# Optimization experiments

Hardware: AMD Instinct MI355X
Metric: run time of the kernel (lower is better)

## Reference

```python
import jax, jax.numpy as jnp
import numpy as np

GATE_DECAY = 3.0

def setup_inputs() -> dict:
    key = jax.random.key(0)
    ks = jax.random.split(key, 4)
    B, S, D, I = 8, 2048, 512, 2048
    x = jax.random.normal(ks[0], (B, S, D), dtype=jnp.float32)
    # kaiming normal fan_in, linear gain: std = 1/sqrt(fan_in)
    Wa = jax.random.normal(ks[1], (I, D), dtype=jnp.float32) / np.sqrt(D)
    Wi = jax.random.normal(ks[2], (I, D), dtype=jnp.float32) / np.sqrt(D)
    ba = jnp.zeros((I,), dtype=jnp.float32)
    bi = jnp.zeros((I,), dtype=jnp.float32)
    lo, hi = np.log(0.9 / 0.1), np.log(0.999 / 0.001)  # logit(0.9), logit(0.999)
    gate = jax.random.uniform(ks[3], (I,), dtype=jnp.float32, minval=lo, maxval=hi)
    return {"x": x, "Wa": Wa, "ba": ba, "Wi": Wi, "bi": bi, "gate": gate}

def reference(x, Wa, ba, Wi, bi, gate):
    # Precompute both projections for all timesteps as large GEMMs.
    pa = jnp.einsum('bsd,id->bsi', x, Wa) + ba   # [B,S,I]
    pi = jnp.einsum('bsd,id->bsi', x, Wi) + bi   # [B,S,I]
    reset_gate = jax.nn.sigmoid(pa)
    input_gate = jax.nn.sigmoid(pi)
    alpha = jax.nn.sigmoid(gate)                  # [I]
    adaptive_alpha = alpha / (GATE_DECAY ** reset_gate)          # [B,S,I]
    drive = jnp.sqrt(1.0 - adaptive_alpha ** 2) * (input_gate * pi)
    B, S, I = pa.shape

    def step(h, ac):
        a, c = ac
        h = a * h + c
        return h, h

    h0 = jnp.zeros((B, I), dtype=x.dtype)
    # scan over time: move S to leading axis
    _, ys = jax.lax.scan(step, h0, (adaptive_alpha.transpose(1, 0, 2), drive.transpose(1, 0, 2)))
    return ys.transpose(1, 0, 2)  # [B,S,I]
```

## Files before the change

### kernel.cpp

```cpp
#include <hip/hip_runtime.h>


#define LOG2_3 1.5849625007211562f

typedef _Float16 f16x8 __attribute__((ext_vector_type(8)));
typedef _Float16 f16x4 __attribute__((ext_vector_type(4)));
typedef _Float16 f16x2 __attribute__((ext_vector_type(2)));
typedef float f32x4 __attribute__((ext_vector_type(4)));

__device__ __forceinline__ float sigmoidf_(float v) {
  return 1.0f / (1.0f + __expf(-v));
}

__device__ __forceinline__ void async_copy16(void* lds, const void* gp) {
  __builtin_amdgcn_global_load_lds((__attribute__((address_space(1))) void*)gp,
                                   (__attribute__((address_space(3))) void*)lds,
                                   16, 0, 0);
}

__global__ __launch_bounds__(256) void cvt_all(const float* __restrict__ x,
                                               const float* __restrict__ Wa,
                                               const float* __restrict__ Wi,
                                               _Float16* __restrict__ xh,
                                               _Float16* __restrict__ wh) {
  int idx = blockIdx.x * 256 + threadIdx.x;
  const float* src;
  _Float16* dst;
  int off, doff;
  if (idx < 2097152) {
    src = x; dst = xh; off = idx; doff = idx;
  } else if (idx < 2097152 + 262144) {
    src = Wa; dst = wh; off = idx - 2097152;
    doff = off + ((off >> 7) << 7);
  } else {
    src = Wi; dst = wh; off = idx - 2359296;
    doff = off + ((off >> 7) << 7) + 128;
  }
  float4 v = ((const float4*)src)[off];
  f16x4 h;
  h[0] = (_Float16)v.x;
  h[1] = (_Float16)v.y;
  h[2] = (_Float16)v.z;
  h[3] = (_Float16)v.w;
  ((f16x4*)dst)[doff] = h;
}

__device__ __forceinline__ void gate_ac(float pa, float pi, float alpha, float& a, float& c) {
  float rg = sigmoidf_(pa);
  a = alpha * exp2f(-LOG2_3 * rg);
  float ig = sigmoidf_(pi);
  c = sqrtf(fmaxf(1.0f - a * a, 0.0f)) * (ig * pi);
}

__global__ __launch_bounds__(256) void gemm_gate(const _Float16* __restrict__ Ah,
                                                 const _Float16* __restrict__ Wh,
                                                 const float* __restrict__ ba,
                                                 const float* __restrict__ bi,
                                                 const float* __restrict__ gate,
                                                 _Float16* __restrict__ AC,
                                                 float2* __restrict__ agg) {
  constexpr int K = 512;
  constexpr int N2 = 4096;
  __shared__ __align__(16) _Float16 smem[8704];
  __shared__ float pAs[8 * 65];
  __shared__ float pHs[8 * 65];
  _Float16* As = smem;
  _Float16* Bs = smem + 4096;
  const int t = threadIdx.x;
  const int mBase = blockIdx.y * 128;
  const int nBase = blockIdx.x * 128;
  const int r = t >> 2;
  const int c8 = (t & 3) * 8;
  const _Float16* gA0 = Ah + (size_t)(mBase + r) * K + c8;
  const _Float16* gB0 = Wh + (size_t)(nBase + r) * K + c8;
  _Float16* lA0 = As + r * 32 + c8;
  _Float16* lB0 = Bs + r * 32 + c8;

  const int lane = t & 63;
  const int wave = t >> 6;
  const int wm = (wave & 1) * 64;
  const int wn = (wave >> 1) * 64;
  const int lrow = lane & 15;
  const int quad = lane >> 4;

  f32x4 acc[4][4];
#pragma unroll
  for (int i = 0; i < 4; ++i)
#pragma unroll
    for (int j = 0; j < 4; ++j)
      acc[i][j] = (f32x4)0.0f;

  for (int kt = 0; kt < K; kt += 32) {
    async_copy16(lA0, gA0 + kt);
    async_copy16(lA0 + 64 * 32, gA0 + (size_t)64 * K + kt);
    async_copy16(lB0, gB0 + kt);
    async_copy16(lB0 + 64 * 32, gB0 + (size_t)64 * K + kt);
    __syncthreads();
    f16x8 af[4], bf[4];
#pragma unroll
    for (int i = 0; i < 4; ++i)
      af[i] = *(const f16x8*)(As + (wm + i * 16 + lrow) * 32 + quad * 8);
#pragma unroll
    for (int j = 0; j < 4; ++j)
      bf[j] = *(const f16x8*)(Bs + (wn + j * 16 + lrow) * 32 + quad * 8);
#pragma unroll
    for (int i = 0; i < 4; ++i)
#pragma unroll
      for (int j = 0; j < 4; ++j)
        acc[i][j] = __builtin_amdgcn_mfma_f32_16x16x32_f16(af[i], bf[j], acc[i][j], 0, 0, 0);
    __syncthreads();
  }

  float bias[4];
#pragma unroll
  for (int j = 0; j < 4; ++j) {
    const int n = nBase + wn + j * 16 + lrow;
    bias[j] = (n & 1) ? bi[n >> 1] : ba[n >> 1];
  }

  const int col = t & 63;
  const int q = t >> 6;
  const float alpha = sigmoidf_(gate[(nBase >> 1) + col]);
  const int b = blockIdx.y >> 4;

#pragma unroll
  for (int h = 0; h < 2; ++h) {
    if (wm == h * 64) {
#pragma unroll
      for (int i = 0; i < 4; ++i)
#pragma unroll
        for (int j = 0; j < 4; ++j)
#pragma unroll
          for (int rr = 0; rr < 4; ++rr)
            smem[(i * 16 + quad * 4 + rr) * 136 + wn + j * 16 + lrow] =
                (_Float16)(acc[i][j][rr] + bias[j]);
    }
    __syncthreads();
    float A = 1.0f, Hn = 0.0f;
    _Float16* ACp = AC + (size_t)(mBase + h * 64 + q * 16) * N2 + nBase + 2 * col;
#pragma unroll 4
    for (int rs = 0; rs < 16; ++rs) {
      f16x2 pp = *(const f16x2*)(smem + (q * 16 + rs) * 136 + 2 * col);
      float a, c;
      gate_ac((float)pp[0], (float)pp[1], alpha, a, c);
      f16x2 o;
      o[0] = (_Float16)a;
      o[1] = (_Float16)c;
      *(f16x2*)ACp = o;
      ACp += N2;
      A *= a;
      Hn = fmaf(a, Hn, c);
    }
    pAs[(h * 4 + q) * 65 + col] = A;
    pHs[(h * 4 + q) * 65 + col] = Hn;
    __syncthreads();
  }

  if (t < 64) {
#pragma unroll
    for (int k = 0; k < 4; ++k) {
      float A0 = pAs[(2 * k) * 65 + t], H0 = pHs[(2 * k) * 65 + t];
      float A1 = pAs[(2 * k + 1) * 65 + t], H1 = pHs[(2 * k + 1) * 65 + t];
      const int ch = ((blockIdx.y & 15) << 2) + k;
      agg[((size_t)(b * 64 + ch)) * 2048 + (nBase >> 1) + t] =
          make_float2(A0 * A1, fmaf(A1, H0, H1));
    }
  }
}

__global__ __launch_bounds__(64) void scan_pass2(const float2* __restrict__ agg,
                                                 float* __restrict__ carry) {
  const int i = blockIdx.x * 64 + threadIdx.x;
  const int b = blockIdx.y;
  float h = 0.0f;
  for (int c8 = 0; c8 < 8; ++c8) {
    float2 aH[8];
#pragma unroll
    for (int u = 0; u < 8; ++u)
      aH[u] = agg[((size_t)(b * 64 + c8 * 8 + u)) * 2048 + i];
#pragma unroll
    for (int u = 0; u < 8; ++u) {
      carry[((size_t)(b * 64 + c8 * 8 + u)) * 2048 + i] = h;
      h = fmaf(aH[u].x, h, aH[u].y);
    }
  }
}

__global__ __launch_bounds__(256) void scan_out(const _Float16* __restrict__ AC,
                                                const float* __restrict__ carry,
                                                float* __restrict__ out) {
  const int tt = blockIdx.x * 256 + threadIdx.x;
  const int i0 = tt * 2;
  const int ch = blockIdx.y;
  const int b = blockIdx.z;
  const float2 cr = ((const float2*)(carry + ((size_t)(b * 64 + ch)) * 2048))[tt];
  float h0 = cr.x, h1 = cr.y;
  const _Float16* row = AC + ((size_t)(b * 2048 + ch * 32)) * 4096 + i0 * 2;
  float* orow = out + ((size_t)(b * 2048 + ch * 32)) * 2048 + i0;
  for (int s4 = 0; s4 < 8; ++s4) {
    f16x4 v[4];
#pragma unroll
    for (int u = 0; u < 4; ++u)
      v[u] = *(const f16x4*)(row + (size_t)u * 4096);
    row += 4 * 4096;
#pragma unroll
    for (int u = 0; u < 4; ++u) {
      h0 = fmaf((float)v[u][0], h0, (float)v[u][1]);
      h1 = fmaf((float)v[u][2], h1, (float)v[u][3]);
      float2 o;
      o.x = h0;
      o.y = h1;
      *(float2*)(orow + (size_t)u * 2048) = o;
    }
    orow += 4 * 2048;
  }
}

extern "C" void kernel_launch(void* const* d_in, const int* in_sizes, int n_in,
                              void* d_out, int out_size, void* d_ws, size_t ws_size,
                              hipStream_t stream) {
  const float* x = (const float*)d_in[0];
  const float* Wa = (const float*)d_in[1];
  const float* ba = (const float*)d_in[2];
  const float* Wi = (const float*)d_in[3];
  const float* bi = (const float*)d_in[4];
  const float* gate = (const float*)d_in[5];
  float* out = (float*)d_out;

  char* ws = (char*)d_ws;
  _Float16* xh = (_Float16*)ws;
  _Float16* wh = (_Float16*)(ws + 16777216);
  const size_t MN2 = (size_t)16384 * 4096;
  _Float16* AC = (_Float16*)(ws + 20971520);
  float2* agg = (float2*)(ws + 20971520 + MN2 * 2);
  float* carry = (float*)(ws + 20971520 + MN2 * 2 + 8388608);

  cvt_all<<<10240, 256, 0, stream>>>(x, Wa, Wi, xh, wh);
  gemm_gate<<<dim3(32, 128), 256, 0, stream>>>(xh, wh, ba, bi, gate, AC, agg);
  scan_pass2<<<dim3(32, 8), 64, 0, stream>>>(agg, carry);
  scan_out<<<dim3(4, 64, 8), 256, 0, stream>>>(AC, carry, out);
}
```

Measured before the change: 357.9 us.

## Double-buffer GEMM LDS tiles with XOR swizzle and widen scan_out vectors

The GEMM main loop now double-buffers its A/B tiles in LDS, so the global-to-LDS async copies for the next K-slice are issued while the current slice is being multiplied. The initial sync before compute is removed. A row-dependent XOR swizzle on 16-byte chunks is meant to cut LDS bank conflicts on the fragment reads. Separately, scan_out processes four channels per thread with 16-byte loads and stores and launches half as many blocks. Costs: LDS use doubles, which may lower occupancy, and correctness relies on async copy completion ordering at the single end-of-iteration barrier.

```diff
diff --git a/kernel.cpp b/kernel.cpp
--- a/kernel.cpp
+++ b/kernel.cpp
@@ -61,20 +61,18 @@
                                                  float2* __restrict__ agg) {
   constexpr int K = 512;
   constexpr int N2 = 4096;
-  __shared__ __align__(16) _Float16 smem[8704];
+  __shared__ __align__(16) _Float16 smem[16384];
   __shared__ float pAs[8 * 65];
   __shared__ float pHs[8 * 65];
-  _Float16* As = smem;
-  _Float16* Bs = smem + 4096;
   const int t = threadIdx.x;
   const int mBase = blockIdx.y * 128;
   const int nBase = blockIdx.x * 128;
   const int r = t >> 2;
-  const int c8 = (t & 3) * 8;
-  const _Float16* gA0 = Ah + (size_t)(mBase + r) * K + c8;
-  const _Float16* gB0 = Wh + (size_t)(nBase + r) * K + c8;
-  _Float16* lA0 = As + r * 32 + c8;
-  _Float16* lB0 = Bs + r * 32 + c8;
+  const int p = t & 3;
+  const int lsw = p ^ ((r >> 1) & 3);
+  const _Float16* gA0 = Ah + (size_t)(mBase + r) * K + lsw * 8;
+  const _Float16* gB0 = Wh + (size_t)(nBase + r) * K + lsw * 8;
+  const int ldst = r * 32 + p * 8;
 
   const int lane = t & 63;
   const int wave = t >> 6;
@@ -82,6 +80,7 @@
   const int wn = (wave >> 1) * 64;
   const int lrow = lane & 15;
   const int quad = lane >> 4;
+  const int xq = quad ^ ((lrow >> 1) & 3);
 
   f32x4 acc[4][4];
 #pragma unroll
@@ -90,19 +89,33 @@
     for (int j = 0; j < 4; ++j)
       acc[i][j] = (f32x4)0.0f;
 
-  for (int kt = 0; kt < K; kt += 32) {
-    async_copy16(lA0, gA0 + kt);
-    async_copy16(lA0 + 64 * 32, gA0 + (size_t)64 * K + kt);
-    async_copy16(lB0, gB0 + kt);
-    async_copy16(lB0 + 64 * 32, gB0 + (size_t)64 * K + kt);
-    __syncthreads();
+  _Float16* b0 = smem;
+  _Float16* b1 = smem + 8192;
+
+  async_copy16(b0 + ldst, gA0);
+  async_copy16(b0 + 2048 + ldst, gA0 + (size_t)64 * K);
+  async_copy16(b0 + 4096 + ldst, gB0);
+  async_copy16(b0 + 6144 + ldst, gB0 + (size_t)64 * K);
+  __syncthreads();
+
+#pragma unroll
+  for (int kt = 0; kt < 16; ++kt) {
+    _Float16* cur = (kt & 1) ? b1 : b0;
+    _Float16* nxt = (kt & 1) ? b0 : b1;
+    if (kt < 15) {
+      const int ko = (kt + 1) * 32;
+      async_copy16(nxt + ldst, gA0 + ko);
+      async_copy16(nxt + 2048 + ldst, gA0 + (size_t)64 * K + ko);
+      async_copy16(nxt + 4096 + ldst, gB0 + ko);
+      async_copy16(nxt + 6144 + ldst, gB0 + (size_t)64 * K + ko);
+    }
     f16x8 af[4], bf[4];
 #pragma unroll
     for (int i = 0; i < 4; ++i)
-      af[i] = *(const f16x8*)(As + (wm + i * 16 + lrow) * 32 + quad * 8);
+      af[i] = *(const f16x8*)(cur + (wm + i * 16 + lrow) * 32 + xq * 8);
 #pragma unroll
     for (int j = 0; j < 4; ++j)
-      bf[j] = *(const f16x8*)(Bs + (wn + j * 16 + lrow) * 32 + quad * 8);
+      bf[j] = *(const f16x8*)(cur + 4096 + (wn + j * 16 + lrow) * 32 + xq * 8);
 #pragma unroll
     for (int i = 0; i < 4; ++i)
 #pragma unroll
@@ -190,27 +203,31 @@
                                                 const float* __restrict__ carry,
                                                 float* __restrict__ out) {
   const int tt = blockIdx.x * 256 + threadIdx.x;
-  const int i0 = tt * 2;
+  const int i0 = tt * 4;
   const int ch = blockIdx.y;
   const int b = blockIdx.z;
-  const float2 cr = ((const float2*)(carry + ((size_t)(b * 64 + ch)) * 2048))[tt];
-  float h0 = cr.x, h1 = cr.y;
+  const float4 cr = ((const float4*)(carry + ((size_t)(b * 64 + ch)) * 2048))[tt];
+  float h0 = cr.x, h1 = cr.y, h2 = cr.z, h3 = cr.w;
   const _Float16* row = AC + ((size_t)(b * 2048 + ch * 32)) * 4096 + i0 * 2;
   float* orow = out + ((size_t)(b * 2048 + ch * 32)) * 2048 + i0;
   for (int s4 = 0; s4 < 8; ++s4) {
-    f16x4 v[4];
+    f16x8 v[4];
 #pragma unroll
     for (int u = 0; u < 4; ++u)
-      v[u] = *(const f16x4*)(row + (size_t)u * 4096);
+      v[u] = *(const f16x8*)(row + (size_t)u * 4096);
     row += 4 * 4096;
 #pragma unroll
     for (int u = 0; u < 4; ++u) {
       h0 = fmaf((float)v[u][0], h0, (float)v[u][1]);
       h1 = fmaf((float)v[u][2], h1, (float)v[u][3]);
-      float2 o;
+      h2 = fmaf((float)v[u][4], h2, (float)v[u][5]);
+      h3 = fmaf((float)v[u][6], h3, (float)v[u][7]);
+      float4 o;
       o.x = h0;
       o.y = h1;
-      *(float2*)(orow + (size_t)u * 2048) = o;
+      o.z = h2;
+      o.w = h3;
+      *(float4*)(orow + (size_t)u * 2048) = o;
     }
     orow += 4 * 2048;
   }
@@ -238,5 +255,5 @@
   cvt_all<<<10240, 256, 0, stream>>>(x, Wa, Wi, xh, wh);
   gemm_gate<<<dim3(32, 128), 256, 0, stream>>>(xh, wh, ba, bi, gate, AC, agg);
   scan_pass2<<<dim3(32, 8), 64, 0, stream>>>(agg, carry);
-  scan_out<<<dim3(4, 64, 8), 256, 0, stream>>>(AC, carry, out);
-}
+  scan_out<<<dim3(2, 64, 8), 256, 0, stream>>>(AC, carry, out);
+}
```

Result: faster. 344.1 us (-3.9%).
